# Kernel optimization log

Hardware: AMD Instinct MI355X
Metric: run time of the kernel (lower is better)

Reference implementation:

```python
import jax, jax.numpy as jnp
import numpy as np

EPS = 1e-06
SCALING = 1.0
P_NORM = 1  # p for Wasserstein
N_PROJ = 100


def setup_inputs() -> dict:
    key = jax.random.key(0)
    k1, k2, k3 = jax.random.split(key, 3)
    # uniform(0,1): all pixels strictly positive, matching the module's x>0 mask densely
    X = jax.random.uniform(k1, (8, 3, 128, 128), dtype=jnp.float32)
    Y = jax.random.uniform(k2, (8, 3, 128, 128), dtype=jnp.float32)
    # raw gaussian projections; normalized to unit columns inside reference (as POT does)
    projections = jax.random.normal(k3, (2, N_PROJ), dtype=jnp.float32)
    return {"X": X, "Y": Y, "projections": projections}


def _quantiles(cws, qs, xs_sorted):
    # cws: (n, P) cumulative weights; qs: (m, P) query levels; xs_sorted: (n, P)
    idx = jax.vmap(lambda c, q: jnp.searchsorted(c, q), in_axes=1, out_axes=1)(cws, qs)
    return jnp.take_along_axis(xs_sorted, jnp.clip(idx, 0, xs_sorted.shape[0] - 1), axis=0)


def reference(X, Y, projections):
    B, C, H, W = X.shape
    HW = H * W

    # --- eps safeguard: if max of (b, channel 0) < eps, bump its argmax to eps ---
    flat = X.reshape(B, C, HW)
    max_vals = flat.max(axis=-1)            # (B, C)
    max_inds = flat.argmax(axis=-1)         # (B, C)
    should_max = max_vals[:, 0] < EPS       # (B,)
    b_idx = jnp.arange(B)
    cur = flat[b_idx, 0, max_inds[:, 0]]
    flat = flat.at[b_idx, 0, max_inds[:, 0]].set(jnp.where(should_max, EPS, cur))
    X = flat.reshape(B, C, H, W)

    Xm = X.mean(axis=1)   # (B, H, W) -- channel-averaged, as X[b, 0] after keepdim mean
    Yc = Y[:, 0]          # (B, H, W) -- Y uses channel 0 only

    # grid coordinates = torch.nonzero order (row-major (i, j)); all pixels > 0
    ii, jj = jnp.meshgrid(jnp.arange(H), jnp.arange(W), indexing="ij")
    coords = jnp.stack([ii, jj], axis=-1).reshape(HW, 2).astype(X.dtype) / SCALING

    # unit-norm projection directions (POT get_random_projections)
    proj = projections / jnp.linalg.norm(projections, axis=0, keepdims=True)  # (2, P)
    pc = coords @ proj                                  # (HW, P) projected coords
    sorter = jnp.argsort(pc, axis=0)                    # shared across batch (same grid)
    pc_sorted = jnp.take_along_axis(pc, sorter, axis=0)

    # normalized weights (normalize=True): x[x>0] / x.sum()
    wX = Xm.reshape(B, HW)
    wX = wX / wX.sum(axis=-1, keepdims=True)
    wY = Yc.reshape(B, HW)
    wY = wY / wY.sum(axis=-1, keepdims=True)

    def swd(wx, wy):
        # weighted 1D Wasserstein per projection (POT wasserstein_1d, quantile form)
        u_cw = jnp.cumsum(wx[sorter], axis=0)           # (HW, P)
        v_cw = jnp.cumsum(wy[sorter], axis=0)           # (HW, P)
        qs = jnp.sort(jnp.concatenate([u_cw, v_cw], axis=0), axis=0)  # (2HW, P)
        uq = _quantiles(u_cw, qs, pc_sorted)
        vq = _quantiles(v_cw, qs, pc_sorted)
        delta = jnp.diff(qs, axis=0, prepend=jnp.zeros((1, qs.shape[1]), qs.dtype))
        w1 = jnp.sum(delta * jnp.abs(uq - vq) ** P_NORM, axis=0)      # (P,)
        res = w1.mean()
        return res if P_NORM == 1 else res ** (1.0 / P_NORM)

    losses = jax.vmap(swd)(wX, wY)   # (B,)
    return losses.sum()              # module accumulates loss over batch (no reduction applied)
```

## Files before the change

### kernel.cpp

```cpp
#include <hip/hip_runtime.h>
#include <hip/hip_fp16.h>
#include <math.h>

#define HW 16384
#define NPROJ 100
#define NB 8
#define NCH 32
#define CHLEN 512
#define EPSV 1e-6f

__device__ inline float4 add4(float4 a, float4 b) {
    return make_float4(a.x + b.x, a.y + b.y, a.z + b.z, a.w + b.w);
}
__device__ inline float4 sub4(float4 a, float4 b) {
    return make_float4(a.x - b.x, a.y - b.y, a.z - b.z, a.w - b.w);
}
__device__ inline float4 shfl_up4(float4 v, int off) {
    return make_float4(__shfl_up(v.x, off), __shfl_up(v.y, off),
                       __shfl_up(v.z, off), __shfl_up(v.w, off));
}
__device__ inline float4 shfl_up4w(float4 v, int off, int w) {
    return make_float4(__shfl_up(v.x, off, w), __shfl_up(v.y, off, w),
                       __shfl_up(v.z, off, w), __shfl_up(v.w, off, w));
}
__device__ inline unsigned int packh2(float a, float b) {
    __half2 h = __floats2half2_rn(a, b);
    return *reinterpret_cast<unsigned int*>(&h);
}
__device__ inline float2 unpackh2(unsigned int w) {
    __half2 h = *reinterpret_cast<__half2*>(&w);
    return make_float2(__low2float(h), __high2float(h));
}

__global__ __launch_bounds__(256) void partial_kernel(const float* __restrict__ X,
                                                      const float* __restrict__ Y,
                                                      float* __restrict__ Xs,
                                                      float* __restrict__ Pmax,
                                                      int* __restrict__ Pidx,
                                                      float* __restrict__ Psx,
                                                      float* __restrict__ Psy,
                                                      float* __restrict__ out) {
    const int blk = blockIdx.x;
    const int b = blk >> 5, c = blk & 31;
    const int tid = threadIdx.x, lane = tid & 63, wid = tid >> 6;
    if (blk == 0 && tid == 0) out[0] = 0.0f;
    const float* xb = X + (size_t)b * 3 * HW;
    const float* yb = Y + (size_t)b * 3 * HW;
    const int base = c * CHLEN;

    float mv = -INFINITY;
    int mi = 0;
    float sx = 0.0f, sy = 0.0f;
#pragma unroll
    for (int k = 0; k < 2; ++k) {
        int p = base + k * 256 + tid;
        float x0 = xb[p], x1 = xb[HW + p], x2 = xb[2 * HW + p], y0 = yb[p];
        float s = x0 + x1 + x2;
        Xs[(size_t)b * HW + p] = s;
        sx += s;
        sy += y0;
        if (x0 > mv) { mv = x0; mi = p; }
    }
#pragma unroll
    for (int off = 32; off > 0; off >>= 1) {
        float ov = __shfl_down(mv, off);
        int oi = __shfl_down(mi, off);
        sx += __shfl_down(sx, off);
        sy += __shfl_down(sy, off);
        if (ov > mv || (ov == mv && oi < mi)) { mv = ov; mi = oi; }
    }
    __shared__ float lmv[4], lsx[4], lsy[4];
    __shared__ int lmi[4];
    if (lane == 0) { lmv[wid] = mv; lmi[wid] = mi; lsx[wid] = sx; lsy[wid] = sy; }
    __syncthreads();
    if (tid == 0) {
        for (int w = 1; w < 4; ++w) {
            if (lmv[w] > lmv[0] || (lmv[w] == lmv[0] && lmi[w] < lmi[0])) {
                lmv[0] = lmv[w];
                lmi[0] = lmi[w];
            }
            lsx[0] += lsx[w];
            lsy[0] += lsy[w];
        }
        Pmax[blk] = lmv[0];
        Pidx[blk] = lmi[0];
        Psx[blk] = lsx[0];
        Psy[blk] = lsy[0];
    }
}

__global__ __launch_bounds__(256) void zprep_kernel(const float* __restrict__ Pmax,
                                                    const int* __restrict__ Pidx,
                                                    const float* __restrict__ Psx,
                                                    const float* __restrict__ Psy,
                                                    const float* __restrict__ Xs,
                                                    const float* __restrict__ Y,
                                                    uint4* __restrict__ Zh) {
    __shared__ float sInvX[8], sInvY[8], sFa[8];
    __shared__ int sFi[8];
    const int tid = threadIdx.x;
    const int c = tid & 31;
    {
        const int b = tid >> 5;
        float mv = Pmax[tid];
        int mi = Pidx[tid];
        float sx = Psx[tid];
        float sy = Psy[tid];
#pragma unroll
        for (int off = 16; off > 0; off >>= 1) {
            float ov = __shfl_down(mv, off, 32);
            int oi = __shfl_down(mi, off, 32);
            float osx = __shfl_down(sx, off, 32);
            float osy = __shfl_down(sy, off, 32);
            if (ov > mv || (ov == mv && oi < mi)) { mv = ov; mi = oi; }
            sx += osx;
            sy += osy;
        }
        if (c == 0) {
            float fa = (mv < EPSV) ? (EPSV - mv) : 0.0f;
            sFa[b] = fa;
            sFi[b] = mi;
            sInvX[b] = 1.0f / (sx + fa);
            sInvY[b] = 1.0f / sy;
        }
    }
    __syncthreads();
    const int p = blockIdx.x * 256 + tid;
    float z[8];
#pragma unroll
    for (int b = 0; b < 8; ++b) {
        float s = Xs[(size_t)b * HW + p];
        if (p == sFi[b]) s += sFa[b];
        z[b] = s * sInvX[b] - Y[(size_t)b * 3 * HW + p] * sInvY[b];
    }
    Zh[p] = make_uint4(packh2(z[0], z[1]), packh2(z[2], z[3]),
                       packh2(z[4], z[5]), packh2(z[6], z[7]));
}

__global__ __launch_bounds__(1024)
__attribute__((amdgpu_waves_per_eu(4, 4)))
void wproj_kernel(const float* __restrict__ proj,
                  const uint4* __restrict__ Zh,
                  float* __restrict__ out) {
    __shared__ int ce[255];
    __shared__ unsigned short Ptab[256 * 128];
    __shared__ int psum[8 * 128];
    __shared__ unsigned short sidT[8192];
    __shared__ float4 lwa[17], lwb[17];
    __shared__ float lred[16];
    __shared__ int sBound;
    __shared__ int sAnyTie;

    const int jp = blockIdx.x >> 1;
    const int h = blockIdx.x & 1;
    const int tid = threadIdx.x, lane = tid & 63, wid = tid >> 6;
    float a = proj[jp];
    float b = proj[NPROJ + jp];
    float inv = 1.0f / sqrtf(a * a + b * b);
    const float an = a * inv, bn = b * inv;
    const float ap = fabsf(an), bp = fabsf(bn);
    const bool flipi = (an < 0.0f), flipj = (bn < 0.0f);

    if (bp == 0.0f) {
        for (int t = tid; t < HW; t += 1024) {
            int i2 = t >> 7, j2 = t & 127;
            int ii = flipi ? 127 - i2 : i2;
            int jj = flipj ? 127 - j2 : j2;
            int idv = ii * 128 + jj;
            if (t == 8192) sBound = idv;
            int q = t - (h << 13);
            if ((unsigned)q < 8192u)
                sidT[(q & 7) * 1024 + (q >> 3)] = (unsigned short)idv;
        }
        __syncthreads();
    } else {
        if (tid == 0) sAnyTie = 0;
        if (tid < 255) {
            int d = tid - 127;
            double v = (double)d * ((double)ap / (double)bp);
            double cv = ceil(v);
            int e = (cv == v) ? 1 : 0;
            int c = (int)fmin(fmax(cv, -128.0), 129.0);
            ce[tid] = c * 2 + e;
            if (e && d >= 1) sAnyTie = 1;
        }
        __syncthreads();

        const int j2 = tid & 127;
        const int g = tid >> 7;
        const int jj = flipj ? 127 - j2 : j2;
        const bool anyTie = (sAnyTie != 0);

        int lp[32];
        int tmask = 0;
        {
            int run = 0;
            const int dd0 = g * 32;
#pragma unroll
            for (int q = 0; q < 32; ++q) {
                int dd = dd0 + q;
                int cl = 0;
                if (dd < 255) {
                    int c = ce[dd] >> 1;
                    cl = min(max(c + j2, 0), 128);
                }
                run += cl;
                lp[q] = run;
            }
            int tcnt = 0;
            if (anyTie) {
#pragma unroll
                for (int q = 1; q <= 16; ++q) {
                    int i2p = g * 16 + q;
                    if (i2p <= 127) {
                        int v = ce[i2p + 127];
                        if (v & 1) {
                            int tj = j2 + (v >> 1);
                            if (tj >= 0 && tj < 128) { tmask |= (1 << q); tcnt++; }
                        }
                    }
                }
            }
            psum[g * 128 + j2] = (run << 5) | tcnt;
        }
        __syncthreads();

        int carryP = 0, carryT = 0;
        for (int g2 = 0; g2 < g; ++g2) {
            int v = psum[g2 * 128 + j2];
            carryP += (v >> 5);
            carryT += (v & 31);
        }
        if (g == 0) Ptab[j2] = 0;
        {
            const int dd0 = g * 32;
#pragma unroll
            for (int q = 0; q < 32; ++q) {
                int dd = dd0 + q;
                if (dd < 255)
                    Ptab[(dd + 1) * 128 + j2] = (unsigned short)(carryP + lp[q]);
            }
        }
        __syncthreads();

        int tsum = carryT;
        const int i2s = g * 16;
#pragma unroll
        for (int q = 0; q < 16; ++q) {
            int i2 = i2s + q;
            if (q > 0) tsum += (tmask >> q) & 1;
            int wsum = (int)Ptab[(i2 + 128) * 128 + j2] - (int)Ptab[i2 * 128 + j2];
            int pos = wsum + tsum;
            int ii = flipi ? 127 - i2 : i2;
            int idv = ii * 128 + jj;
            if (pos == 8192) sBound = idv;
            int ql = pos - (h << 13);
            if ((unsigned)ql < 8192u)
                sidT[(ql & 7) * 1024 + (ql >> 3)] = (unsigned short)idv;
        }
        __syncthreads();
    }

    int ids[9];
#pragma unroll
    for (int m = 0; m < 8; ++m) ids[m] = (int)sidT[m * 1024 + tid];
    ids[8] = (tid < 1023) ? (int)sidT[tid + 1]
                          : ((h == 0) ? sBound : ids[7]);

    float dpc[8];
    {
        float pc_cur = (float)(ids[0] >> 7) * an + (float)(ids[0] & 127) * bn;
#pragma unroll
        for (int m = 0; m < 8; ++m) {
            int idn = ids[m + 1];
            float pc_nxt = (float)(idn >> 7) * an + (float)(idn & 127) * bn;
            dpc[m] = pc_nxt - pc_cur;
            pc_cur = pc_nxt;
        }
    }

    float4 zva[8], zvb[8];
#pragma unroll
    for (int m = 0; m < 8; ++m) {
        uint4 r = Zh[ids[m]];
        float2 f0 = unpackh2(r.x);
        float2 f1 = unpackh2(r.y);
        float2 f2 = unpackh2(r.z);
        float2 f3 = unpackh2(r.w);
        zva[m] = make_float4(f0.x, f0.y, f1.x, f1.y);
        zvb[m] = make_float4(f2.x, f2.y, f3.x, f3.y);
    }
#pragma unroll
    for (int m = 1; m < 8; ++m) {
        zva[m] = add4(zva[m], zva[m - 1]);
        zvb[m] = add4(zvb[m], zvb[m - 1]);
    }
    const float4 tota = zva[7], totb = zvb[7];

    float4 ia = tota, ib = totb;
#pragma unroll
    for (int off = 1; off < 64; off <<= 1) {
        float4 ua = shfl_up4(ia, off);
        float4 ub = shfl_up4(ib, off);
        if (lane >= off) { ia = add4(ia, ua); ib = add4(ib, ub); }
    }
    if (lane == 63) { lwa[wid] = ia; lwb[wid] = ib; }
    __syncthreads();
    if (tid < 16) {
        float4 va = lwa[tid], vb = lwb[tid];
        float4 sa = va, sb = vb;
#pragma unroll
        for (int off = 1; off < 16; off <<= 1) {
            float4 ua = shfl_up4w(sa, off, 16);
            float4 ub = shfl_up4w(sb, off, 16);
            if (tid >= off) { sa = add4(sa, ua); sb = add4(sb, ub); }
        }
        lwa[tid] = sub4(sa, va);
        lwb[tid] = sub4(sb, vb);
        if (tid == 15) { lwa[16] = sa; lwb[16] = sb; }
    }
    __syncthreads();

    float4 preA = add4(sub4(ia, tota), lwa[wid]);
    float4 preB = add4(sub4(ib, totb), lwb[wid]);
    if (h == 1) {
        preA = sub4(preA, lwa[16]);
        preB = sub4(preB, lwb[16]);
    }

    float acc = 0.0f;
#pragma unroll
    for (int m = 0; m < 8; ++m) {
        float4 cxa = add4(preA, zva[m]);
        float4 cxb = add4(preB, zvb[m]);
        float s8 = fabsf(cxa.x) + fabsf(cxa.y) + fabsf(cxa.z) + fabsf(cxa.w)
                 + fabsf(cxb.x) + fabsf(cxb.y) + fabsf(cxb.z) + fabsf(cxb.w);
        acc += s8 * dpc[m];
    }

#pragma unroll
    for (int off = 32; off > 0; off >>= 1) acc += __shfl_down(acc, off);
    if (lane == 0) lred[wid] = acc;
    __syncthreads();
    if (tid == 0) {
        float r = 0.0f;
        for (int w = 0; w < 16; ++w) r += lred[w];
        atomicAdd(out, r * (1.0f / NPROJ));
    }
}

extern "C" void kernel_launch(void* const* d_in, const int* in_sizes, int n_in,
                              void* d_out, int out_size, void* d_ws, size_t ws_size,
                              hipStream_t stream) {
    const float* X = (const float*)d_in[0];
    const float* Y = (const float*)d_in[1];
    const float* proj = (const float*)d_in[2];
    float* out = (float*)d_out;

    char* ws = (char*)d_ws;
    size_t off = 0;
    float* Xs = (float*)(ws + off);     off += (size_t)NB * HW * sizeof(float);
    uint4* Zh = (uint4*)(ws + off);     off += (size_t)HW * sizeof(uint4);
    float* Pmax = (float*)(ws + off);   off += NB * NCH * sizeof(float);
    int* Pidx = (int*)(ws + off);       off += NB * NCH * sizeof(int);
    float* Psx = (float*)(ws + off);    off += NB * NCH * sizeof(float);
    float* Psy = (float*)(ws + off);    off += NB * NCH * sizeof(float);

    partial_kernel<<<NB * NCH, 256, 0, stream>>>(X, Y, Xs, Pmax, Pidx, Psx, Psy, out);
    zprep_kernel<<<HW / 256, 256, 0, stream>>>(Pmax, Pidx, Psx, Psy, Xs, Y, Zh);
    wproj_kernel<<<NPROJ * 2, 1024, 0, stream>>>(proj, Zh, out);
}
```

Measured before the change: 26.20 us.

## Fuse three kernels into one cooperative kernel with grid-wide syncs

Merges the partial-reduction, normalization/z-prep and projection kernels into a single cooperative launch of 200 blocks of 1024 threads, using grid.sync() between phases. The per-projection sort/index setup is overlapped with the preprocessing, since the second grid sync is placed after the sidT construction. The goal is to remove two kernel launches and their inter-kernel gaps. The cost is two grid-wide barriers, a slower cooperative launch path, and the large-LDS, 1024-thread blocks all having to be co-resident.

```diff
diff --git a/kernel.cpp b/kernel.cpp
--- a/kernel.cpp
+++ b/kernel.cpp
@@ -1,12 +1,13 @@
 #include <hip/hip_runtime.h>
+#include <hip/hip_cooperative_groups.h>
 #include <hip/hip_fp16.h>
 #include <math.h>
+
+namespace cg = cooperative_groups;
 
 #define HW 16384
 #define NPROJ 100
 #define NB 8
-#define NCH 32
-#define CHLEN 512
 #define EPSV 1e-6f
 
 __device__ inline float4 add4(float4 a, float4 b) {
@@ -32,115 +33,17 @@
     return make_float2(__low2float(h), __high2float(h));
 }
 
-__global__ __launch_bounds__(256) void partial_kernel(const float* __restrict__ X,
-                                                      const float* __restrict__ Y,
-                                                      float* __restrict__ Xs,
-                                                      float* __restrict__ Pmax,
-                                                      int* __restrict__ Pidx,
-                                                      float* __restrict__ Psx,
-                                                      float* __restrict__ Psy,
-                                                      float* __restrict__ out) {
-    const int blk = blockIdx.x;
-    const int b = blk >> 5, c = blk & 31;
-    const int tid = threadIdx.x, lane = tid & 63, wid = tid >> 6;
-    if (blk == 0 && tid == 0) out[0] = 0.0f;
-    const float* xb = X + (size_t)b * 3 * HW;
-    const float* yb = Y + (size_t)b * 3 * HW;
-    const int base = c * CHLEN;
-
-    float mv = -INFINITY;
-    int mi = 0;
-    float sx = 0.0f, sy = 0.0f;
-#pragma unroll
-    for (int k = 0; k < 2; ++k) {
-        int p = base + k * 256 + tid;
-        float x0 = xb[p], x1 = xb[HW + p], x2 = xb[2 * HW + p], y0 = yb[p];
-        float s = x0 + x1 + x2;
-        Xs[(size_t)b * HW + p] = s;
-        sx += s;
-        sy += y0;
-        if (x0 > mv) { mv = x0; mi = p; }
-    }
-#pragma unroll
-    for (int off = 32; off > 0; off >>= 1) {
-        float ov = __shfl_down(mv, off);
-        int oi = __shfl_down(mi, off);
-        sx += __shfl_down(sx, off);
-        sy += __shfl_down(sy, off);
-        if (ov > mv || (ov == mv && oi < mi)) { mv = ov; mi = oi; }
-    }
-    __shared__ float lmv[4], lsx[4], lsy[4];
-    __shared__ int lmi[4];
-    if (lane == 0) { lmv[wid] = mv; lmi[wid] = mi; lsx[wid] = sx; lsy[wid] = sy; }
-    __syncthreads();
-    if (tid == 0) {
-        for (int w = 1; w < 4; ++w) {
-            if (lmv[w] > lmv[0] || (lmv[w] == lmv[0] && lmi[w] < lmi[0])) {
-                lmv[0] = lmv[w];
-                lmi[0] = lmi[w];
-            }
-            lsx[0] += lsx[w];
-            lsy[0] += lsy[w];
-        }
-        Pmax[blk] = lmv[0];
-        Pidx[blk] = lmi[0];
-        Psx[blk] = lsx[0];
-        Psy[blk] = lsy[0];
-    }
-}
-
-__global__ __launch_bounds__(256) void zprep_kernel(const float* __restrict__ Pmax,
-                                                    const int* __restrict__ Pidx,
-                                                    const float* __restrict__ Psx,
-                                                    const float* __restrict__ Psy,
-                                                    const float* __restrict__ Xs,
-                                                    const float* __restrict__ Y,
-                                                    uint4* __restrict__ Zh) {
-    __shared__ float sInvX[8], sInvY[8], sFa[8];
-    __shared__ int sFi[8];
-    const int tid = threadIdx.x;
-    const int c = tid & 31;
-    {
-        const int b = tid >> 5;
-        float mv = Pmax[tid];
-        int mi = Pidx[tid];
-        float sx = Psx[tid];
-        float sy = Psy[tid];
-#pragma unroll
-        for (int off = 16; off > 0; off >>= 1) {
-            float ov = __shfl_down(mv, off, 32);
-            int oi = __shfl_down(mi, off, 32);
-            float osx = __shfl_down(sx, off, 32);
-            float osy = __shfl_down(sy, off, 32);
-            if (ov > mv || (ov == mv && oi < mi)) { mv = ov; mi = oi; }
-            sx += osx;
-            sy += osy;
-        }
-        if (c == 0) {
-            float fa = (mv < EPSV) ? (EPSV - mv) : 0.0f;
-            sFa[b] = fa;
-            sFi[b] = mi;
-            sInvX[b] = 1.0f / (sx + fa);
-            sInvY[b] = 1.0f / sy;
-        }
-    }
-    __syncthreads();
-    const int p = blockIdx.x * 256 + tid;
-    float z[8];
-#pragma unroll
-    for (int b = 0; b < 8; ++b) {
-        float s = Xs[(size_t)b * HW + p];
-        if (p == sFi[b]) s += sFa[b];
-        z[b] = s * sInvX[b] - Y[(size_t)b * 3 * HW + p] * sInvY[b];
-    }
-    Zh[p] = make_uint4(packh2(z[0], z[1]), packh2(z[2], z[3]),
-                       packh2(z[4], z[5]), packh2(z[6], z[7]));
-}
-
 __global__ __launch_bounds__(1024)
 __attribute__((amdgpu_waves_per_eu(4, 4)))
-void wproj_kernel(const float* __restrict__ proj,
-                  const uint4* __restrict__ Zh,
+void fused_kernel(const float* __restrict__ X,
+                  const float* __restrict__ Y,
+                  const float* __restrict__ proj,
+                  float* __restrict__ Xs,
+                  uint4* __restrict__ Zh,
+                  float* __restrict__ Pmax,
+                  int* __restrict__ Pidx,
+                  float* __restrict__ Psx,
+                  float* __restrict__ Psy,
                   float* __restrict__ out) {
     __shared__ int ce[255];
     __shared__ unsigned short Ptab[256 * 128];
@@ -148,12 +51,98 @@
     __shared__ unsigned short sidT[8192];
     __shared__ float4 lwa[17], lwb[17];
     __shared__ float lred[16];
+    __shared__ float lmv[16], lsx[16], lsy[16];
+    __shared__ int lmi[16];
+    __shared__ float sInvX[8], sInvY[8], sFa[8];
+    __shared__ int sFi[8];
     __shared__ int sBound;
     __shared__ int sAnyTie;
 
-    const int jp = blockIdx.x >> 1;
-    const int h = blockIdx.x & 1;
+    cg::grid_group grid = cg::this_grid();
+    const int bid = blockIdx.x;
     const int tid = threadIdx.x, lane = tid & 63, wid = tid >> 6;
+
+    if (bid == 0 && tid == 0) out[0] = 0.0f;
+    if (bid < 128) {
+        const int b = bid >> 4;
+        const int p = (bid & 15) * 1024 + tid;
+        const float* xb = X + (size_t)b * 3 * HW;
+        float x0 = xb[p], x1 = xb[HW + p], x2 = xb[2 * HW + p];
+        float y0 = Y[(size_t)b * 3 * HW + p];
+        float s = x0 + x1 + x2;
+        Xs[(size_t)b * HW + p] = s;
+        float mv = x0;
+        int mi = p;
+        float sx = s, sy = y0;
+#pragma unroll
+        for (int off = 32; off > 0; off >>= 1) {
+            float ov = __shfl_down(mv, off);
+            int oi = __shfl_down(mi, off);
+            sx += __shfl_down(sx, off);
+            sy += __shfl_down(sy, off);
+            if (ov > mv || (ov == mv && oi < mi)) { mv = ov; mi = oi; }
+        }
+        if (lane == 0) { lmv[wid] = mv; lmi[wid] = mi; lsx[wid] = sx; lsy[wid] = sy; }
+        __syncthreads();
+        if (tid == 0) {
+            for (int w = 1; w < 16; ++w) {
+                if (lmv[w] > lmv[0] || (lmv[w] == lmv[0] && lmi[w] < lmi[0])) {
+                    lmv[0] = lmv[w];
+                    lmi[0] = lmi[w];
+                }
+                lsx[0] += lsx[w];
+                lsy[0] += lsy[w];
+            }
+            Pmax[bid] = lmv[0];
+            Pidx[bid] = lmi[0];
+            Psx[bid] = lsx[0];
+            Psy[bid] = lsy[0];
+        }
+    }
+    grid.sync();
+
+    if (tid < 128) {
+        const int b = tid >> 4, k = tid & 15;
+        float mv = Pmax[b * 16 + k];
+        int mi = Pidx[b * 16 + k];
+        float sx = Psx[b * 16 + k];
+        float sy = Psy[b * 16 + k];
+#pragma unroll
+        for (int off = 8; off > 0; off >>= 1) {
+            float ov = __shfl_down(mv, off, 16);
+            int oi = __shfl_down(mi, off, 16);
+            float osx = __shfl_down(sx, off, 16);
+            float osy = __shfl_down(sy, off, 16);
+            if (ov > mv || (ov == mv && oi < mi)) { mv = ov; mi = oi; }
+            sx += osx;
+            sy += osy;
+        }
+        if (k == 0) {
+            float fa = (mv < EPSV) ? (EPSV - mv) : 0.0f;
+            sFa[b] = fa;
+            sFi[b] = mi;
+            sInvX[b] = 1.0f / (sx + fa);
+            sInvY[b] = 1.0f / sy;
+        }
+    }
+    __syncthreads();
+    {
+        const int p = bid * 82 + tid;
+        if (tid < 82 && p < HW) {
+            float z[8];
+#pragma unroll
+            for (int b = 0; b < 8; ++b) {
+                float s = Xs[(size_t)b * HW + p];
+                if (p == sFi[b]) s += sFa[b];
+                z[b] = s * sInvX[b] - Y[(size_t)b * 3 * HW + p] * sInvY[b];
+            }
+            Zh[p] = make_uint4(packh2(z[0], z[1]), packh2(z[2], z[3]),
+                               packh2(z[4], z[5]), packh2(z[6], z[7]));
+        }
+    }
+
+    const int jp = bid >> 1;
+    const int h = bid & 1;
     float a = proj[jp];
     float b = proj[NPROJ + jp];
     float inv = 1.0f / sqrtf(a * a + b * b);
@@ -261,6 +250,8 @@
         __syncthreads();
     }
 
+    grid.sync();
+
     int ids[9];
 #pragma unroll
     for (int m = 0; m < 8; ++m) ids[m] = (int)sidT[m * 1024 + tid];
@@ -359,14 +350,16 @@
 
     char* ws = (char*)d_ws;
     size_t off = 0;
-    float* Xs = (float*)(ws + off);     off += (size_t)NB * HW * sizeof(float);
-    uint4* Zh = (uint4*)(ws + off);     off += (size_t)HW * sizeof(uint4);
-    float* Pmax = (float*)(ws + off);   off += NB * NCH * sizeof(float);
-    int* Pidx = (int*)(ws + off);       off += NB * NCH * sizeof(int);
-    float* Psx = (float*)(ws + off);    off += NB * NCH * sizeof(float);
-    float* Psy = (float*)(ws + off);    off += NB * NCH * sizeof(float);
-
-    partial_kernel<<<NB * NCH, 256, 0, stream>>>(X, Y, Xs, Pmax, Pidx, Psx, Psy, out);
-    zprep_kernel<<<HW / 256, 256, 0, stream>>>(Pmax, Pidx, Psx, Psy, Xs, Y, Zh);
-    wproj_kernel<<<NPROJ * 2, 1024, 0, stream>>>(proj, Zh, out);
-}
+    float* Xs = (float*)(ws + off);    off += (size_t)NB * HW * sizeof(float);
+    uint4* Zh = (uint4*)(ws + off);    off += (size_t)HW * sizeof(uint4);
+    float* Pmax = (float*)(ws + off);  off += 128 * sizeof(float);
+    int* Pidx = (int*)(ws + off);      off += 128 * sizeof(int);
+    float* Psx = (float*)(ws + off);   off += 128 * sizeof(float);
+    float* Psy = (float*)(ws + off);   off += 128 * sizeof(float);
+
+    void* args[] = {(void*)&X, (void*)&Y, (void*)&proj, (void*)&Xs, (void*)&Zh,
+                    (void*)&Pmax, (void*)&Pidx, (void*)&Psx, (void*)&Psy,
+                    (void*)&out};
+    hipLaunchCooperativeKernel((void*)fused_kernel, dim3(NPROJ * 2), dim3(1024),
+                               args, 0, stream);
+}
```

New measurement: 78.48 us. 3x slower.

## Replace shared prefix table with register-held partial sums in rank computation

Applied to the files above, without the earlier changes.

The 64KB Ptab shared-memory prefix table and the ce lookup array are removed. Each thread now computes ceil boundaries in double precision directly for two 16-row segments, keeps both running sums in registers, and builds carries from a doubled psum array, which drops one barrier and the table writes and reads. In exchange each thread does twice as many double-precision ceil computations, and register pressure rises under the fixed waves-per-eu setting. The much smaller LDS footprint could allow more blocks per CU.

```diff
diff --git a/kernel.cpp b/kernel.cpp
--- a/kernel.cpp
+++ b/kernel.cpp
@@ -142,14 +142,11 @@
 void wproj_kernel(const float* __restrict__ proj,
                   const uint4* __restrict__ Zh,
                   float* __restrict__ out) {
-    __shared__ int ce[255];
-    __shared__ unsigned short Ptab[256 * 128];
-    __shared__ int psum[8 * 128];
+    __shared__ int psum[16 * 128];
     __shared__ unsigned short sidT[8192];
     __shared__ float4 lwa[17], lwb[17];
     __shared__ float lred[16];
     __shared__ int sBound;
-    __shared__ int sAnyTie;
 
     const int jp = blockIdx.x >> 1;
     const int h = blockIdx.x & 1;
@@ -174,74 +171,61 @@
         }
         __syncthreads();
     } else {
-        if (tid == 0) sAnyTie = 0;
-        if (tid < 255) {
-            int d = tid - 127;
-            double v = (double)d * ((double)ap / (double)bp);
-            double cv = ceil(v);
-            int e = (cv == v) ? 1 : 0;
-            int c = (int)fmin(fmax(cv, -128.0), 129.0);
-            ce[tid] = c * 2 + e;
-            if (e && d >= 1) sAnyTie = 1;
-        }
-        __syncthreads();
-
         const int j2 = tid & 127;
         const int g = tid >> 7;
         const int jj = flipj ? 127 - j2 : j2;
-        const bool anyTie = (sAnyTie != 0);
-
-        int lp[32];
-        int tmask = 0;
+        const double r = (double)ap / (double)bp;
+
+        int lpA[16], lpB[16];
+        int tmask = 0, tcnt = 0;
         {
-            int run = 0;
-            const int dd0 = g * 32;
-#pragma unroll
-            for (int q = 0; q < 32; ++q) {
-                int dd = dd0 + q;
-                int cl = 0;
-                if (dd < 255) {
-                    int c = ce[dd] >> 1;
-                    cl = min(max(c + j2, 0), 128);
+            int runA = 0, runB = 0;
+            const int ddA0 = g * 16;
+            const int ddB0 = g * 16 + 128;
+#pragma unroll
+            for (int q = 0; q < 16; ++q) {
+                {
+                    int d = ddA0 + q - 127;
+                    double v = (double)d * r;
+                    double cv = ceil(v);
+                    int c = (int)fmin(fmax(cv, -128.0), 129.0);
+                    runA += min(max(c + j2, 0), 128);
+                    lpA[q] = runA;
                 }
-                run += cl;
-                lp[q] = run;
-            }
-            int tcnt = 0;
-            if (anyTie) {
-#pragma unroll
-                for (int q = 1; q <= 16; ++q) {
-                    int i2p = g * 16 + q;
-                    if (i2p <= 127) {
-                        int v = ce[i2p + 127];
-                        if (v & 1) {
-                            int tj = j2 + (v >> 1);
-                            if (tj >= 0 && tj < 128) { tmask |= (1 << q); tcnt++; }
+                {
+                    int dd = ddB0 + q;
+                    int cl = 0;
+                    if (dd < 255) {
+                        int d = dd - 127;
+                        double v = (double)d * r;
+                        double cv = ceil(v);
+                        int c = (int)fmin(fmax(cv, -128.0), 129.0);
+                        cl = min(max(c + j2, 0), 128);
+                        if (cv == v && d <= 127) {
+                            int tj = j2 + c;
+                            if (tj >= 0 && tj < 128) {
+                                tmask |= (1 << (q + 1));
+                                tcnt++;
+                            }
                         }
                     }
+                    runB += cl;
+                    lpB[q] = runB;
                 }
             }
-            psum[g * 128 + j2] = (run << 5) | tcnt;
+            psum[g * 128 + j2] = runA << 5;
+            psum[(g + 8) * 128 + j2] = (runB << 5) | tcnt;
         }
         __syncthreads();
 
-        int carryP = 0, carryT = 0;
-        for (int g2 = 0; g2 < g; ++g2) {
-            int v = psum[g2 * 128 + j2];
-            carryP += (v >> 5);
-            carryT += (v & 31);
-        }
-        if (g == 0) Ptab[j2] = 0;
-        {
-            const int dd0 = g * 32;
-#pragma unroll
-            for (int q = 0; q < 32; ++q) {
-                int dd = dd0 + q;
-                if (dd < 255)
-                    Ptab[(dd + 1) * 128 + j2] = (unsigned short)(carryP + lp[q]);
-            }
-        }
-        __syncthreads();
+        int carryA = 0, carryB = 0, carryT = 0;
+        for (int rr = 0; rr < g + 8; ++rr) {
+            int v = psum[rr * 128 + j2];
+            int run = v >> 5;
+            carryB += run;
+            if (rr < g) carryA += run;
+            if (rr >= 8) carryT += (v & 31);
+        }
 
         int tsum = carryT;
         const int i2s = g * 16;
@@ -249,8 +233,9 @@
         for (int q = 0; q < 16; ++q) {
             int i2 = i2s + q;
             if (q > 0) tsum += (tmask >> q) & 1;
-            int wsum = (int)Ptab[(i2 + 128) * 128 + j2] - (int)Ptab[i2 * 128 + j2];
-            int pos = wsum + tsum;
+            int PA = carryA + (q > 0 ? lpA[q - 1] : 0);
+            int PB = carryB + (q > 0 ? lpB[q - 1] : 0);
+            int pos = (PB - PA) + tsum;
             int ii = flipi ? 127 - i2 : i2;
             int idv = ii * 128 + jj;
             if (pos == 8192) sBound = idv;
@@ -282,11 +267,11 @@
     float4 zva[8], zvb[8];
 #pragma unroll
     for (int m = 0; m < 8; ++m) {
-        uint4 r = Zh[ids[m]];
-        float2 f0 = unpackh2(r.x);
-        float2 f1 = unpackh2(r.y);
-        float2 f2 = unpackh2(r.z);
-        float2 f3 = unpackh2(r.w);
+        uint4 rr = Zh[ids[m]];
+        float2 f0 = unpackh2(rr.x);
+        float2 f1 = unpackh2(rr.y);
+        float2 f2 = unpackh2(rr.z);
+        float2 f3 = unpackh2(rr.w);
         zva[m] = make_float4(f0.x, f0.y, f1.x, f1.y);
         zvb[m] = make_float4(f2.x, f2.y, f3.x, f3.y);
     }
@@ -343,9 +328,9 @@
     if (lane == 0) lred[wid] = acc;
     __syncthreads();
     if (tid == 0) {
-        float r = 0.0f;
-        for (int w = 0; w < 16; ++w) r += lred[w];
-        atomicAdd(out, r * (1.0f / NPROJ));
+        float r2 = 0.0f;
+        for (int w = 0; w < 16; ++w) r2 += lred[w];
+        atomicAdd(out, r2 * (1.0f / NPROJ));
     }
 }
 
```

After: 27.62 us. 1.05x slower.

## Fuse prep kernels and defer normalization into the projection kernel

Applied to the files above, without the earlier changes.

Merges the partial-reduction and z-prep kernels into one prep kernel that writes raw half-precision channel sums and Y values plus per-block partials. The final reduction, normalization and eps-fix handling move into the projection kernel, which applies the inverse sums when it gathers each element and corrects for the eps bump by computing its sorted rank. This removes one kernel launch and one pass through global memory. In exchange every projection block redoes the small reduction and gathers twice as many bytes per element, and the values are rounded to fp16 before normalization, which changes precision.

```diff
diff --git a/kernel.cpp b/kernel.cpp
--- a/kernel.cpp
+++ b/kernel.cpp
@@ -5,8 +5,6 @@
 #define HW 16384
 #define NPROJ 100
 #define NB 8
-#define NCH 32
-#define CHLEN 512
 #define EPSV 1e-6f
 
 __device__ inline float4 add4(float4 a, float4 b) {
@@ -14,6 +12,9 @@
 }
 __device__ inline float4 sub4(float4 a, float4 b) {
     return make_float4(a.x - b.x, a.y - b.y, a.z - b.z, a.w - b.w);
+}
+__device__ inline float4 mul4(float4 a, float4 b) {
+    return make_float4(a.x * b.x, a.y * b.y, a.z * b.z, a.w * b.w);
 }
 __device__ inline float4 shfl_up4(float4 v, int off) {
     return make_float4(__shfl_up(v.x, off), __shfl_up(v.y, off),
@@ -32,115 +33,76 @@
     return make_float2(__low2float(h), __high2float(h));
 }
 
-__global__ __launch_bounds__(256) void partial_kernel(const float* __restrict__ X,
-                                                      const float* __restrict__ Y,
-                                                      float* __restrict__ Xs,
-                                                      float* __restrict__ Pmax,
-                                                      int* __restrict__ Pidx,
-                                                      float* __restrict__ Psx,
-                                                      float* __restrict__ Psy,
-                                                      float* __restrict__ out) {
+__global__ __launch_bounds__(256) void prep_kernel(const float* __restrict__ X,
+                                                   const float* __restrict__ Y,
+                                                   uint4* __restrict__ Zraw,
+                                                   float* __restrict__ Pmax,
+                                                   int* __restrict__ Pidx,
+                                                   float* __restrict__ Psx,
+                                                   float* __restrict__ Psy,
+                                                   float* __restrict__ out) {
     const int blk = blockIdx.x;
-    const int b = blk >> 5, c = blk & 31;
     const int tid = threadIdx.x, lane = tid & 63, wid = tid >> 6;
+    const int p = blk * 256 + tid;
     if (blk == 0 && tid == 0) out[0] = 0.0f;
-    const float* xb = X + (size_t)b * 3 * HW;
-    const float* yb = Y + (size_t)b * 3 * HW;
-    const int base = c * CHLEN;
-
-    float mv = -INFINITY;
-    int mi = 0;
-    float sx = 0.0f, sy = 0.0f;
-#pragma unroll
-    for (int k = 0; k < 2; ++k) {
-        int p = base + k * 256 + tid;
-        float x0 = xb[p], x1 = xb[HW + p], x2 = xb[2 * HW + p], y0 = yb[p];
-        float s = x0 + x1 + x2;
-        Xs[(size_t)b * HW + p] = s;
-        sx += s;
-        sy += y0;
-        if (x0 > mv) { mv = x0; mi = p; }
-    }
-#pragma unroll
-    for (int off = 32; off > 0; off >>= 1) {
-        float ov = __shfl_down(mv, off);
-        int oi = __shfl_down(mi, off);
-        sx += __shfl_down(sx, off);
-        sy += __shfl_down(sy, off);
-        if (ov > mv || (ov == mv && oi < mi)) { mv = ov; mi = oi; }
-    }
-    __shared__ float lmv[4], lsx[4], lsy[4];
-    __shared__ int lmi[4];
-    if (lane == 0) { lmv[wid] = mv; lmi[wid] = mi; lsx[wid] = sx; lsy[wid] = sy; }
-    __syncthreads();
-    if (tid == 0) {
+
+    float xs[8], yy[8], x0v[8];
+#pragma unroll
+    for (int b = 0; b < 8; ++b) {
+        const float* xb = X + (size_t)b * 3 * HW;
+        float x0 = xb[p], x1 = xb[HW + p], x2 = xb[2 * HW + p];
+        x0v[b] = x0;
+        xs[b] = x0 + x1 + x2;
+        yy[b] = Y[(size_t)b * 3 * HW + p];
+    }
+    Zraw[2 * p] = make_uint4(packh2(xs[0], xs[1]), packh2(xs[2], xs[3]),
+                             packh2(yy[0], yy[1]), packh2(yy[2], yy[3]));
+    Zraw[2 * p + 1] = make_uint4(packh2(xs[4], xs[5]), packh2(xs[6], xs[7]),
+                                 packh2(yy[4], yy[5]), packh2(yy[6], yy[7]));
+
+    __shared__ float smv[8][4], ssx[8][4], ssy[8][4];
+    __shared__ int smi[8][4];
+#pragma unroll
+    for (int b = 0; b < 8; ++b) {
+        float mv = x0v[b], sx = xs[b], sy = yy[b];
+        int mi = p;
+#pragma unroll
+        for (int off = 32; off > 0; off >>= 1) {
+            float ov = __shfl_down(mv, off);
+            int oi = __shfl_down(mi, off);
+            sx += __shfl_down(sx, off);
+            sy += __shfl_down(sy, off);
+            if (ov > mv || (ov == mv && oi < mi)) { mv = ov; mi = oi; }
+        }
+        if (lane == 0) { smv[b][wid] = mv; smi[b][wid] = mi;
+                         ssx[b][wid] = sx; ssy[b][wid] = sy; }
+    }
+    __syncthreads();
+    if (tid < 8) {
+        float mv = smv[tid][0], sx = ssx[tid][0], sy = ssy[tid][0];
+        int mi = smi[tid][0];
         for (int w = 1; w < 4; ++w) {
-            if (lmv[w] > lmv[0] || (lmv[w] == lmv[0] && lmi[w] < lmi[0])) {
-                lmv[0] = lmv[w];
-                lmi[0] = lmi[w];
-            }
-            lsx[0] += lsx[w];
-            lsy[0] += lsy[w];
-        }
-        Pmax[blk] = lmv[0];
-        Pidx[blk] = lmi[0];
-        Psx[blk] = lsx[0];
-        Psy[blk] = lsy[0];
-    }
-}
-
-__global__ __launch_bounds__(256) void zprep_kernel(const float* __restrict__ Pmax,
-                                                    const int* __restrict__ Pidx,
-                                                    const float* __restrict__ Psx,
-                                                    const float* __restrict__ Psy,
-                                                    const float* __restrict__ Xs,
-                                                    const float* __restrict__ Y,
-                                                    uint4* __restrict__ Zh) {
-    __shared__ float sInvX[8], sInvY[8], sFa[8];
-    __shared__ int sFi[8];
-    const int tid = threadIdx.x;
-    const int c = tid & 31;
-    {
-        const int b = tid >> 5;
-        float mv = Pmax[tid];
-        int mi = Pidx[tid];
-        float sx = Psx[tid];
-        float sy = Psy[tid];
-#pragma unroll
-        for (int off = 16; off > 0; off >>= 1) {
-            float ov = __shfl_down(mv, off, 32);
-            int oi = __shfl_down(mi, off, 32);
-            float osx = __shfl_down(sx, off, 32);
-            float osy = __shfl_down(sy, off, 32);
+            float ov = smv[tid][w];
+            int oi = smi[tid][w];
             if (ov > mv || (ov == mv && oi < mi)) { mv = ov; mi = oi; }
-            sx += osx;
-            sy += osy;
-        }
-        if (c == 0) {
-            float fa = (mv < EPSV) ? (EPSV - mv) : 0.0f;
-            sFa[b] = fa;
-            sFi[b] = mi;
-            sInvX[b] = 1.0f / (sx + fa);
-            sInvY[b] = 1.0f / sy;
-        }
-    }
-    __syncthreads();
-    const int p = blockIdx.x * 256 + tid;
-    float z[8];
-#pragma unroll
-    for (int b = 0; b < 8; ++b) {
-        float s = Xs[(size_t)b * HW + p];
-        if (p == sFi[b]) s += sFa[b];
-        z[b] = s * sInvX[b] - Y[(size_t)b * 3 * HW + p] * sInvY[b];
-    }
-    Zh[p] = make_uint4(packh2(z[0], z[1]), packh2(z[2], z[3]),
-                       packh2(z[4], z[5]), packh2(z[6], z[7]));
+            sx += ssx[tid][w];
+            sy += ssy[tid][w];
+        }
+        Pmax[tid * 64 + blk] = mv;
+        Pidx[tid * 64 + blk] = mi;
+        Psx[tid * 64 + blk] = sx;
+        Psy[tid * 64 + blk] = sy;
+    }
 }
 
 __global__ __launch_bounds__(1024)
 __attribute__((amdgpu_waves_per_eu(4, 4)))
 void wproj_kernel(const float* __restrict__ proj,
-                  const uint4* __restrict__ Zh,
+                  const uint4* __restrict__ Zraw,
+                  const float* __restrict__ Pmax,
+                  const int* __restrict__ Pidx,
+                  const float* __restrict__ Psx,
+                  const float* __restrict__ Psy,
                   float* __restrict__ out) {
     __shared__ int ce[255];
     __shared__ unsigned short Ptab[256 * 128];
@@ -148,8 +110,9 @@
     __shared__ unsigned short sidT[8192];
     __shared__ float4 lwa[17], lwb[17];
     __shared__ float lred[16];
-    __shared__ int sBound;
-    __shared__ int sAnyTie;
+    __shared__ float sInvX[8], sInvY[8], sFa[8];
+    __shared__ int sFi[8], sRfi[8];
+    __shared__ int sBound, sAnyTie, sAnyFix;
 
     const int jp = blockIdx.x >> 1;
     const int h = blockIdx.x & 1;
@@ -160,6 +123,51 @@
     const float an = a * inv, bn = b * inv;
     const float ap = fabsf(an), bp = fabsf(bn);
     const bool flipi = (an < 0.0f), flipj = (bn < 0.0f);
+
+    if (tid == 1023) { sAnyTie = 0; sAnyFix = 0; sBound = 0; }
+    __syncthreads();
+
+    if (tid < 512) {
+        const int b2 = wid, c = lane;
+        float mv = Pmax[b2 * 64 + c];
+        int mi = Pidx[b2 * 64 + c];
+        float sx = Psx[b2 * 64 + c];
+        float sy = Psy[b2 * 64 + c];
+#pragma unroll
+        for (int off = 32; off > 0; off >>= 1) {
+            float ov = __shfl_down(mv, off);
+            int oi = __shfl_down(mi, off);
+            float osx = __shfl_down(sx, off);
+            float osy = __shfl_down(sy, off);
+            if (ov > mv || (ov == mv && oi < mi)) { mv = ov; mi = oi; }
+            sx += osx;
+            sy += osy;
+        }
+        if (c == 0) {
+            float fa = (mv < EPSV) ? (EPSV - mv) : 0.0f;
+            sFa[b2] = fa;
+            sFi[b2] = mi;
+            sInvX[b2] = 1.0f / (sx + fa);
+            sInvY[b2] = 1.0f / sy;
+            if (fa > 0.0f) sAnyFix = 1;
+        }
+    }
+    if (bp != 0.0f && tid >= 512 && tid < 767) {
+        int t = tid - 512;
+        int d = t - 127;
+        double v = (double)d * ((double)ap / (double)bp);
+        double cv = ceil(v);
+        int e = (cv == v) ? 1 : 0;
+        int c = (int)fmin(fmax(cv, -128.0), 129.0);
+        ce[t] = c * 2 + e;
+        if (e && d >= 1) sAnyTie = 1;
+    }
+    __syncthreads();
+
+    const float4 iXa = make_float4(sInvX[0], sInvX[1], sInvX[2], sInvX[3]);
+    const float4 iXb = make_float4(sInvX[4], sInvX[5], sInvX[6], sInvX[7]);
+    const float4 iYa = make_float4(sInvY[0], sInvY[1], sInvY[2], sInvY[3]);
+    const float4 iYb = make_float4(sInvY[4], sInvY[5], sInvY[6], sInvY[7]);
 
     if (bp == 0.0f) {
         for (int t = tid; t < HW; t += 1024) {
@@ -174,18 +182,6 @@
         }
         __syncthreads();
     } else {
-        if (tid == 0) sAnyTie = 0;
-        if (tid < 255) {
-            int d = tid - 127;
-            double v = (double)d * ((double)ap / (double)bp);
-            double cv = ceil(v);
-            int e = (cv == v) ? 1 : 0;
-            int c = (int)fmin(fmax(cv, -128.0), 129.0);
-            ce[tid] = c * 2 + e;
-            if (e && d >= 1) sAnyTie = 1;
-        }
-        __syncthreads();
-
         const int j2 = tid & 127;
         const int g = tid >> 7;
         const int jj = flipj ? 127 - j2 : j2;
@@ -261,6 +257,33 @@
         __syncthreads();
     }
 
+    const bool anyFix = (sAnyFix != 0);
+    if (anyFix) {
+        if (tid < 8) {
+            int fi = sFi[tid];
+            int ii = fi >> 7, jj = fi & 127;
+            int i2 = flipi ? 127 - ii : ii;
+            int j2 = flipj ? 127 - jj : jj;
+            if (bp == 0.0f) {
+                sRfi[tid] = i2 * 128 + j2;
+            } else {
+                int wsum = 0;
+                for (int dd = i2; dd < i2 + 128; ++dd)
+                    wsum += min(max((ce[dd] >> 1) + j2, 0), 128);
+                int tsum = 0;
+                for (int i2p = 1; i2p <= i2; ++i2p) {
+                    int v = ce[i2p + 127];
+                    if (v & 1) {
+                        int tj = j2 + (v >> 1);
+                        if (tj >= 0 && tj < 128) tsum++;
+                    }
+                }
+                sRfi[tid] = wsum + tsum;
+            }
+        }
+        __syncthreads();
+    }
+
     int ids[9];
 #pragma unroll
     for (int m = 0; m < 8; ++m) ids[m] = (int)sidT[m * 1024 + tid];
@@ -282,13 +305,18 @@
     float4 zva[8], zvb[8];
 #pragma unroll
     for (int m = 0; m < 8; ++m) {
-        uint4 r = Zh[ids[m]];
-        float2 f0 = unpackh2(r.x);
-        float2 f1 = unpackh2(r.y);
-        float2 f2 = unpackh2(r.z);
-        float2 f3 = unpackh2(r.w);
-        zva[m] = make_float4(f0.x, f0.y, f1.x, f1.y);
-        zvb[m] = make_float4(f2.x, f2.y, f3.x, f3.y);
+        uint4 r0 = Zraw[2 * ids[m]];
+        uint4 r1 = Zraw[2 * ids[m] + 1];
+        float2 x01 = unpackh2(r0.x), x23 = unpackh2(r0.y);
+        float2 y01 = unpackh2(r0.z), y23 = unpackh2(r0.w);
+        float2 x45 = unpackh2(r1.x), x67 = unpackh2(r1.y);
+        float2 y45 = unpackh2(r1.z), y67 = unpackh2(r1.w);
+        float4 xsA = make_float4(x01.x, x01.y, x23.x, x23.y);
+        float4 ysA = make_float4(y01.x, y01.y, y23.x, y23.y);
+        float4 xsB = make_float4(x45.x, x45.y, x67.x, x67.y);
+        float4 ysB = make_float4(y45.x, y45.y, y67.x, y67.y);
+        zva[m] = sub4(mul4(xsA, iXa), mul4(ysA, iYa));
+        zvb[m] = sub4(mul4(xsB, iXb), mul4(ysB, iYb));
     }
 #pragma unroll
     for (int m = 1; m < 8; ++m) {
@@ -326,16 +354,42 @@
     if (h == 1) {
         preA = sub4(preA, lwa[16]);
         preB = sub4(preB, lwb[16]);
+        if (anyFix) {
+            preA = sub4(preA, make_float4(sFa[0] * sInvX[0], sFa[1] * sInvX[1],
+                                          sFa[2] * sInvX[2], sFa[3] * sInvX[3]));
+            preB = sub4(preB, make_float4(sFa[4] * sInvX[4], sFa[5] * sInvX[5],
+                                          sFa[6] * sInvX[6], sFa[7] * sInvX[7]));
+        }
     }
 
     float acc = 0.0f;
-#pragma unroll
-    for (int m = 0; m < 8; ++m) {
-        float4 cxa = add4(preA, zva[m]);
-        float4 cxb = add4(preB, zvb[m]);
-        float s8 = fabsf(cxa.x) + fabsf(cxa.y) + fabsf(cxa.z) + fabsf(cxa.w)
-                 + fabsf(cxb.x) + fabsf(cxb.y) + fabsf(cxb.z) + fabsf(cxb.w);
-        acc += s8 * dpc[m];
+    if (!anyFix) {
+#pragma unroll
+        for (int m = 0; m < 8; ++m) {
+            float4 cxa = add4(preA, zva[m]);
+            float4 cxb = add4(preB, zvb[m]);
+            float s8 = fabsf(cxa.x) + fabsf(cxa.y) + fabsf(cxa.z) + fabsf(cxa.w)
+                     + fabsf(cxb.x) + fabsf(cxb.y) + fabsf(cxb.z) + fabsf(cxb.w);
+            acc += s8 * dpc[m];
+        }
+    } else {
+#pragma unroll
+        for (int m = 0; m < 8; ++m) {
+            float4 cxa = add4(preA, zva[m]);
+            float4 cxb = add4(preB, zvb[m]);
+            int gpos = (h << 13) + tid * 8 + m;
+            if (gpos >= sRfi[0]) cxa.x += sFa[0] * sInvX[0];
+            if (gpos >= sRfi[1]) cxa.y += sFa[1] * sInvX[1];
+            if (gpos >= sRfi[2]) cxa.z += sFa[2] * sInvX[2];
+            if (gpos >= sRfi[3]) cxa.w += sFa[3] * sInvX[3];
+            if (gpos >= sRfi[4]) cxb.x += sFa[4] * sInvX[4];
+            if (gpos >= sRfi[5]) cxb.y += sFa[5] * sInvX[5];
+            if (gpos >= sRfi[6]) cxb.z += sFa[6] * sInvX[6];
+            if (gpos >= sRfi[7]) cxb.w += sFa[7] * sInvX[7];
+            float s8 = fabsf(cxa.x) + fabsf(cxa.y) + fabsf(cxa.z) + fabsf(cxa.w)
+                     + fabsf(cxb.x) + fabsf(cxb.y) + fabsf(cxb.z) + fabsf(cxb.w);
+            acc += s8 * dpc[m];
+        }
     }
 
 #pragma unroll
@@ -343,9 +397,9 @@
     if (lane == 0) lred[wid] = acc;
     __syncthreads();
     if (tid == 0) {
-        float r = 0.0f;
-        for (int w = 0; w < 16; ++w) r += lred[w];
-        atomicAdd(out, r * (1.0f / NPROJ));
+        float r2 = 0.0f;
+        for (int w = 0; w < 16; ++w) r2 += lred[w];
+        atomicAdd(out, r2 * (1.0f / NPROJ));
     }
 }
 
@@ -359,14 +413,12 @@
 
     char* ws = (char*)d_ws;
     size_t off = 0;
-    float* Xs = (float*)(ws + off);     off += (size_t)NB * HW * sizeof(float);
-    uint4* Zh = (uint4*)(ws + off);     off += (size_t)HW * sizeof(uint4);
-    float* Pmax = (float*)(ws + off);   off += NB * NCH * sizeof(float);
-    int* Pidx = (int*)(ws + off);       off += NB * NCH * sizeof(int);
-    float* Psx = (float*)(ws + off);    off += NB * NCH * sizeof(float);
-    float* Psy = (float*)(ws + off);    off += NB * NCH * sizeof(float);
-
-    partial_kernel<<<NB * NCH, 256, 0, stream>>>(X, Y, Xs, Pmax, Pidx, Psx, Psy, out);
-    zprep_kernel<<<HW / 256, 256, 0, stream>>>(Pmax, Pidx, Psx, Psy, Xs, Y, Zh);
-    wproj_kernel<<<NPROJ * 2, 1024, 0, stream>>>(proj, Zh, out);
-}
+    uint4* Zraw = (uint4*)(ws + off);   off += (size_t)2 * HW * sizeof(uint4);
+    float* Pmax = (float*)(ws + off);   off += NB * 64 * sizeof(float);
+    int* Pidx = (int*)(ws + off);       off += NB * 64 * sizeof(int);
+    float* Psx = (float*)(ws + off);    off += NB * 64 * sizeof(float);
+    float* Psy = (float*)(ws + off);    off += NB * 64 * sizeof(float);
+
+    prep_kernel<<<HW / 256, 256, 0, stream>>>(X, Y, Zraw, Pmax, Pidx, Psx, Psy, out);
+    wproj_kernel<<<NPROJ * 2, 1024, 0, stream>>>(proj, Zraw, Pmax, Pidx, Psx, Psy, out);
+}
```

New measurement: 30.52 us. +16.5%, slower.
